# Optimization experiments

Measured on AMD Instinct MI355X. Metric: run time of the kernel, lower is better.

## Reference

```python
import jax, jax.numpy as jnp
import numpy as np

K = 4  # kNN neighbors


def build_edges(density_maps, k):
    B, _, H, W = density_maps.shape
    N = H * W
    flat = density_maps.reshape(B, N)
    # [B, N, N] pairwise absolute density distance
    dist = jnp.abs(flat[:, :, None] - flat[:, None, :])
    # k nearest (excluding self at position 0)
    tgt = jnp.argsort(dist, axis=2)[:, :, 1:k + 1]  # [B, N, k]
    src = jnp.broadcast_to(jnp.arange(N)[None, :, None], (B, N, k))
    offset = (jnp.arange(B) * N)[:, None, None]
    src = (src + offset).reshape(-1)
    tgt = (tgt + offset).reshape(-1)
    n_total = B * N
    loops = jnp.arange(n_total)
    row = jnp.concatenate([src, loops])  # source nodes
    col = jnp.concatenate([tgt, loops])  # target nodes
    return row, col, n_total


def gcn_conv(x, row, col, W, b, n_nodes):
    # symmetric deg^-1/2 normalization, deg computed on target (col)
    deg = jax.ops.segment_sum(jnp.ones_like(col, dtype=x.dtype), col, num_segments=n_nodes)
    dinv = jnp.where(deg > 0, jax.lax.rsqrt(deg), 0.0)
    norm = dinv[row] * dinv[col]  # [E]
    h = x @ W  # transform first, then propagate
    msg = norm[:, None] * h[row]
    out = jax.ops.segment_sum(msg, col, num_segments=n_nodes)
    return out + b


def setup_inputs() -> dict:
    key = jax.random.key(0)
    k1, k2, k3, k4, k5, k6 = jax.random.split(key, 6)
    B, Cin, Chid, Cout, H, W = 4, 256, 512, 256, 64, 64
    density_maps = jax.random.uniform(k1, (B, 1, H, W), dtype=jnp.float32)
    feature_maps = jax.random.normal(k2, (B, Cin, H, W), dtype=jnp.float32)
    W1 = jax.random.normal(k3, (Cin, Chid), dtype=jnp.float32) * (1.0 / np.sqrt(Cin))
    b1 = jnp.zeros((Chid,), dtype=jnp.float32)
    W2 = jax.random.normal(k4, (Chid, Cout), dtype=jnp.float32) * (1.0 / np.sqrt(Chid))
    b2 = jnp.zeros((Cout,), dtype=jnp.float32)
    return {"density_maps": density_maps, "feature_maps": feature_maps,
            "W1": W1, "b1": b1, "W2": W2, "b2": b2}


def reference(density_maps, feature_maps, W1, b1, W2, b2):
    B, Cin, H, Wd = feature_maps.shape
    row, col, n_total = build_edges(density_maps, K)
    # [B,C,H,W] -> [B*H*W, C] node features
    x = feature_maps.transpose(0, 2, 3, 1).reshape(-1, Cin)
    h = jax.nn.relu(gcn_conv(x, row, col, W1, b1, n_total))
    out = jax.nn.relu(gcn_conv(h, row, col, W2, b2, n_total))
    return out.reshape(B, H, Wd, -1).transpose(0, 3, 1, 2)
```

## Files before the change

kernel.cpp:

```cpp
#include <hip/hip_runtime.h>
#include <hip/hip_bf16.h>
#include <stdint.h>

#define N_NODES 16384
#define NPB     4096
#define NB      4
#define KNN     4
#define WIN     12
#define NBUK    4096

typedef short bf16x8 __attribute__((ext_vector_type(8)));
typedef float f32x4 __attribute__((ext_vector_type(4)));
typedef unsigned short u16x8 __attribute__((ext_vector_type(8)));

__device__ __forceinline__ unsigned short f2bf(float f) {
  unsigned u = __float_as_uint(f);
  unsigned r = (u + 0x7fff + ((u >> 16) & 1)) >> 16;
  return (unsigned short)r;
}
__device__ __forceinline__ float bf2f(unsigned short u) {
  return __uint_as_float(((unsigned)u) << 16);
}

__global__ __launch_bounds__(1024)
void bucket_kernel(const float* __restrict__ dm,
                   unsigned long long* __restrict__ skeys_g,
                   int* __restrict__ rank_g,
                   float* __restrict__ dinv_g,
                   unsigned* __restrict__ mask_g) {
  __shared__ int sHist[4096];
  __shared__ int sCur[4096];
  __shared__ unsigned long long sKeys[4096];
  __shared__ unsigned sMask[4096];
  int* part1 = (int*)sKeys;
  int* part2 = (int*)(sKeys + 512);
  const int t = threadIdx.x, b = blockIdx.x;
  const float* d = dm + b * NPB;

  unsigned long long kv[4]; int bk[4];
#pragma unroll
  for (int r = 0; r < 4; ++r) sHist[t + r * 1024] = 0;
  __syncthreads();
#pragma unroll
  for (int r = 0; r < 4; ++r) {
    int i = t + r * 1024;
    float v = d[i];
    kv[r] = (((unsigned long long)__float_as_uint(v)) << 32) | (unsigned)i;
    int k = (int)(v * (float)NBUK); if (k > NBUK - 1) k = NBUK - 1;
    bk[r] = k;
    atomicAdd(&sHist[k], 1);
  }
  __syncthreads();
  int c0 = sHist[4 * t + 0], c1 = sHist[4 * t + 1];
  int c2 = sHist[4 * t + 2], c3 = sHist[4 * t + 3];
  part1[t] = c0 + c1 + c2 + c3;
  __syncthreads();
  if (t < 64) {
    int s = 0;
#pragma unroll
    for (int k = 0; k < 16; ++k) s += part1[16 * t + k];
    part2[t] = s;
  }
  __syncthreads();
  if (t == 0) {
    int a = 0;
    for (int u = 0; u < 64; ++u) { int v = part2[u]; part2[u] = a; a += v; }
  }
  __syncthreads();
  int base = part2[t >> 4];
  for (int k = (t >> 4) * 16; k < t; ++k) base += part1[k];
  sHist[4 * t + 0] = base; sCur[4 * t + 0] = base; base += c0;
  sHist[4 * t + 1] = base; sCur[4 * t + 1] = base; base += c1;
  sHist[4 * t + 2] = base; sCur[4 * t + 2] = base; base += c2;
  sHist[4 * t + 3] = base; sCur[4 * t + 3] = base;
  __syncthreads();
#pragma unroll
  for (int r = 0; r < 4; ++r) {
    int slot = atomicAdd(&sCur[bk[r]], 1);
    sKeys[slot] = kv[r];
  }
  __syncthreads();
#pragma unroll
  for (int r = 0; r < 4; ++r) {
    int g = t + r * 1024;
    int s0 = sHist[g];
    int s1 = (g == NPB - 1) ? NPB : sHist[g + 1];
    for (int i = s0 + 1; i < s1; ++i) {
      unsigned long long x = sKeys[i];
      int j = i - 1;
      while (j >= s0 && sKeys[j] > x) { sKeys[j + 1] = sKeys[j]; --j; }
      sKeys[j + 1] = x;
    }
  }
  __syncthreads();
#pragma unroll
  for (int r = 0; r < 4; ++r) {
    int i = t + r * 1024;
    sHist[i] = 1;
    sMask[i] = 0;
  }
  __syncthreads();
#pragma unroll
  for (int r = 0; r < 4; ++r) {
    int p = t + r * 1024;
    unsigned long long kp = sKeys[p];
    float di = __uint_as_float((unsigned)(kp >> 32));
    int lo = p - WIN; if (lo < 0) lo = 0;
    int hi = p + WIN; if (hi > NPB - 1) hi = NPB - 1;
    unsigned long long k0 = ~0ull, k1 = ~0ull, k2 = ~0ull, k3 = ~0ull, k4 = ~0ull;
    for (int q = lo; q <= hi; ++q) {
      unsigned long long key = sKeys[q];
      float v = __uint_as_float((unsigned)(key >> 32));
      float dist = fabsf(di - v);
      unsigned long long dk = (((unsigned long long)__float_as_uint(dist)) << 24) |
                              ((key & 0xfffull) << 12) | (unsigned)q;
      if (dk < k4) {
        if (dk < k0)      { k4 = k3; k3 = k2; k2 = k1; k1 = k0; k0 = dk; }
        else if (dk < k1) { k4 = k3; k3 = k2; k2 = k1; k1 = dk; }
        else if (dk < k2) { k4 = k3; k3 = k2; k2 = dk; }
        else if (dk < k3) { k4 = k3; k3 = dk; }
        else              { k4 = dk; }
      }
    }
    int t0 = (int)(k1 & 0xfff), t1 = (int)(k2 & 0xfff);
    int t2 = (int)(k3 & 0xfff), t3 = (int)(k4 & 0xfff);
    atomicAdd(&sHist[t0], 1); atomicOr(&sMask[t0], 1u << (p - t0 + WIN));
    atomicAdd(&sHist[t1], 1); atomicOr(&sMask[t1], 1u << (p - t1 + WIN));
    atomicAdd(&sHist[t2], 1); atomicOr(&sMask[t2], 1u << (p - t2 + WIN));
    atomicAdd(&sHist[t3], 1); atomicOr(&sMask[t3], 1u << (p - t3 + WIN));
  }
  __syncthreads();
#pragma unroll
  for (int r = 0; r < 4; ++r) {
    int i = t + r * 1024;
    unsigned long long k = sKeys[i];
    skeys_g[b * NPB + i] = k;
    rank_g[b * NPB + (int)(k & 0xffffffffull)] = i;
    dinv_g[b * NPB + i] = rsqrtf((float)sHist[i]);
    mask_g[b * NPB + i] = sMask[i];
  }
}

__global__ void cvt_all_kernel(const float* __restrict__ fm, unsigned short* __restrict__ px0,
                               const float* __restrict__ W1, unsigned short* __restrict__ W1t,
                               const float* __restrict__ W2, unsigned short* __restrict__ W2t,
                               const int* __restrict__ rank) {
  __shared__ float tile[64][33];
  int z = blockIdx.z;
  const float* in; unsigned short* outbase; int Rin, Cin, r0, c0;
  bool perm = false;
  if (z < NB) {
    in = fm + (size_t)z * 256 * 4096; outbase = px0 + (size_t)z * NPB * 256;
    Rin = 256; Cin = 4096; perm = true;
    c0 = blockIdx.x * 32; r0 = blockIdx.y * 64;
  } else {
    int id = blockIdx.y * 128 + blockIdx.x;
    if (id < 64)       { in = W1; outbase = W1t; Rin = 256; Cin = 512; c0 = (id & 15) * 32; r0 = (id >> 4) * 64; }
    else if (id < 128) { id -= 64; in = W2; outbase = W2t; Rin = 512; Cin = 256; c0 = (id & 7) * 32; r0 = (id >> 3) * 64; }
    else return;
  }
  int tx = threadIdx.x & 31, ty = threadIdx.x >> 5;
  const float* ip = in + (size_t)(r0 + ty) * Cin + c0 + tx;
#pragma unroll
  for (int i = 0; i < 8; ++i) tile[ty + 8 * i][tx] = ip[(size_t)(8 * i) * Cin];
  __syncthreads();
  int orow = threadIdx.x >> 3;
  int oseg = (threadIdx.x & 7) * 8;
  int outrow = c0 + orow;
  if (perm) outrow = rank[(size_t)z * NPB + outrow];
  unsigned short* op = outbase + (size_t)outrow * Rin + r0 + oseg;
  u16x8 o;
#pragma unroll
  for (int k = 0; k < 8; ++k) o[k] = f2bf(tile[oseg + k][orow]);
  *(u16x8*)op = o;
}

__global__ __launch_bounds__(256)
void transpose64_kernel(const float* __restrict__ in, float* __restrict__ out) {
  __shared__ float tile[64][68];
  int cb = blockIdx.x * 64;
  int nb = blockIdx.y * 64;
  int b = blockIdx.z;
  int r = threadIdx.x >> 2, q = threadIdx.x & 3;
  const float* ip = in + ((size_t)b * NPB + nb + r) * 256 + cb;
#pragma unroll
  for (int it = 0; it < 4; ++it) {
    int c = q * 4 + it * 16;
    *(float4*)&tile[r][c] = *(const float4*)(ip + c);
  }
  __syncthreads();
  float* op = out + ((size_t)b * 256 + cb + r) * 4096 + nb;
#pragma unroll
  for (int it = 0; it < 4; ++it) {
    int n = q * 4 + it * 16;
    float4 v;
    v.x = tile[n + 0][r]; v.y = tile[n + 1][r];
    v.z = tile[n + 2][r]; v.w = tile[n + 3][r];
    *(float4*)(op + n) = v;
  }
}

__global__ void prop_kernel(const unsigned short* __restrict__ in,
                            unsigned short* __restrict__ out,
                            const unsigned* __restrict__ mask,
                            const float* __restrict__ dinv) {
  int i = blockIdx.x * 8 + (threadIdx.x >> 5);
  int l = threadIdx.x & 31;
  unsigned m = mask[i];
  float a[8] = {};
#pragma unroll
  for (int off = 0; off < 2 * WIN + 1; ++off) {
    int c = ((m >> off) & 1) + (off == WIN);
    if (c) {
      int q = i + off - WIN;
      float dj = (float)c * dinv[q];
      u16x8 u = *(const u16x8*)(in + (size_t)q * 256 + l * 8);
#pragma unroll
      for (int k = 0; k < 8; ++k) a[k] = fmaf(dj, bf2f(u[k]), a[k]);
    }
  }
  float di = dinv[i];
  u16x8 o;
#pragma unroll
  for (int k = 0; k < 8; ++k) o[k] = f2bf(a[k] * di);
  *(u16x8*)(out + (size_t)i * 256 + l * 8) = o;
}

__global__ void prop2_kernel(const unsigned short* __restrict__ in,
                             float* __restrict__ out,
                             const unsigned* __restrict__ mask,
                             const float* __restrict__ dinv,
                             const float* __restrict__ bias,
                             const unsigned long long* __restrict__ skeys) {
  int i = blockIdx.x * 8 + (threadIdx.x >> 5);
  int l = threadIdx.x & 31;
  unsigned m = mask[i];
  float a[8] = {};
#pragma unroll
  for (int off = 0; off < 2 * WIN + 1; ++off) {
    int c = ((m >> off) & 1) + (off == WIN);
    if (c) {
      int q = i + off - WIN;
      float dj = (float)c * dinv[q];
      u16x8 u = *(const u16x8*)(in + (size_t)q * 256 + l * 8);
#pragma unroll
      for (int k = 0; k < 8; ++k) a[k] = fmaf(dj, bf2f(u[k]), a[k]);
    }
  }
  float di = dinv[i];
  int node = (i & ~(NPB - 1)) + (int)(skeys[i] & 0xffffffffull);
  float4 o0, o1;
  o0.x = fmaxf(a[0] * di + bias[l * 8 + 0], 0.f);
  o0.y = fmaxf(a[1] * di + bias[l * 8 + 1], 0.f);
  o0.z = fmaxf(a[2] * di + bias[l * 8 + 2], 0.f);
  o0.w = fmaxf(a[3] * di + bias[l * 8 + 3], 0.f);
  o1.x = fmaxf(a[4] * di + bias[l * 8 + 4], 0.f);
  o1.y = fmaxf(a[5] * di + bias[l * 8 + 5], 0.f);
  o1.z = fmaxf(a[6] * di + bias[l * 8 + 6], 0.f);
  o1.w = fmaxf(a[7] * di + bias[l * 8 + 7], 0.f);
  *(float4*)(out + (size_t)node * 256 + l * 8) = o0;
  *(float4*)(out + (size_t)node * 256 + l * 8 + 4) = o1;
}

template <bool BIAS_RELU, bool OUT_BF16, int NI>
__global__ __launch_bounds__(256)
void gemm_bf16_kernel(const unsigned short* __restrict__ A,
                      const unsigned short* __restrict__ Bt,
                      void* __restrict__ C, const float* __restrict__ bias,
                      int M, int N, int K) {
  __shared__ char lds[8192 + NI * 8192];
  const int tid = threadIdx.x;
  const int l = tid & 63, w = tid >> 6;
  const int bm = blockIdx.x * 64, bn = blockIdx.y * (64 * NI);
  f32x4 acc[4][NI] = {};

  for (int k0 = 0; k0 < K; k0 += 64) {
    __syncthreads();
#pragma unroll
    for (int q = 0; q < 2; ++q) {
      int o = q * 4096 + tid * 16;
      int r = o >> 7;
      int gc = ((o >> 4) & 7) ^ (r & 7);
      const char* srcA = (const char*)A + ((size_t)(bm + r) * K + k0) * 2 + gc * 16;
      __builtin_amdgcn_global_load_lds(
          (const __attribute__((address_space(1))) void*)srcA,
          (__attribute__((address_space(3))) void*)(lds + o), 16, 0, 0);
    }
#pragma unroll
    for (int q = 0; q < 2 * NI; ++q) {
      int o = q * 4096 + tid * 16;
      int r = o >> 7;
      int gc = ((o >> 4) & 7) ^ (r & 7);
      const char* srcB = (const char*)Bt + ((size_t)(bn + r) * K + k0) * 2 + gc * 16;
      __builtin_amdgcn_global_load_lds(
          (const __attribute__((address_space(1))) void*)srcB,
          (__attribute__((address_space(3))) void*)(lds + 8192 + o), 16, 0, 0);
    }
    __syncthreads();

#pragma unroll
    for (int kk = 0; kk < 64; kk += 32) {
      bf16x8 af[4], bf[NI];
      int gc = (kk >> 3) + (l >> 4);
#pragma unroll
      for (int mi = 0; mi < 4; ++mi) {
        int r = mi * 16 + (l & 15);
        af[mi] = *(const bf16x8*)(lds + r * 128 + ((gc ^ (r & 7)) << 4));
      }
#pragma unroll
      for (int ni = 0; ni < NI; ++ni) {
        int r = w * (16 * NI) + ni * 16 + (l & 15);
        bf[ni] = *(const bf16x8*)(lds + 8192 + r * 128 + ((gc ^ (r & 7)) << 4));
      }
#pragma unroll
      for (int mi = 0; mi < 4; ++mi)
#pragma unroll
        for (int ni = 0; ni < NI; ++ni)
          acc[mi][ni] = __builtin_amdgcn_mfma_f32_16x16x32_bf16(af[mi], bf[ni],
                                                                acc[mi][ni], 0, 0, 0);
    }
  }

#pragma unroll
  for (int mi = 0; mi < 4; ++mi) {
#pragma unroll
    for (int ni = 0; ni < NI; ++ni) {
      int row0 = bm + mi * 16 + ((l >> 4) << 2);
      int col = bn + w * (16 * NI) + ni * 16 + (l & 15);
      float bv = BIAS_RELU ? bias[col] : 0.f;
      f32x4 v = acc[mi][ni];
#pragma unroll
      for (int r = 0; r < 4; ++r) {
        float val = v[r];
        if (BIAS_RELU) val = fmaxf(val + bv, 0.f);
        if (OUT_BF16)
          ((unsigned short*)C)[(size_t)(row0 + r) * N + col] = f2bf(val);
        else
          ((float*)C)[(size_t)(row0 + r) * N + col] = val;
      }
    }
  }
}

extern "C" void kernel_launch(void* const* d_in, const int* in_sizes, int n_in,
                              void* d_out, int out_size, void* d_ws, size_t ws_size,
                              hipStream_t stream) {
  const float* dm = (const float*)d_in[0];
  const float* fm = (const float*)d_in[1];
  const float* W1 = (const float*)d_in[2];
  const float* b1 = (const float*)d_in[3];
  const float* W2 = (const float*)d_in[4];
  const float* b2 = (const float*)d_in[5];
  float* out = (float*)d_out;

  char* ws = (char*)d_ws;
  float*              dinv  = (float*)(ws + 0x050000);
  unsigned*           mask  = (unsigned*)(ws + 0x060000);
  unsigned long long* skeys = (unsigned long long*)(ws + 0x100000);
  int*                rank  = (int*)(ws + 0x130000);
  unsigned short*     W1t   = (unsigned short*)(ws + 0x190000);
  unsigned short*     W2t   = (unsigned short*)(ws + 0x1D0000);
  unsigned short*     px0   = (unsigned short*)(ws + 0x0400000);
  unsigned short*     px    = (unsigned short*)(ws + 0x0C00000);
  unsigned short*     h1    = (unsigned short*)(ws + 0x1400000);
  unsigned short*     t2    = (unsigned short*)(ws + 0x2400000);
  float*              xout  = (float*)(ws + 0x2C00000);
  (void)ws_size; (void)in_sizes; (void)n_in; (void)out_size;

  bucket_kernel<<<NB, 1024, 0, stream>>>(dm, skeys, rank, dinv, mask);

  cvt_all_kernel<<<dim3(128, 4, NB + 1), 256, 0, stream>>>(fm, px0, W1, W1t, W2, W2t, rank);

  prop_kernel<<<N_NODES / 8, 256, 0, stream>>>(px0, px, mask, dinv);
  gemm_bf16_kernel<true, true, 1><<<dim3(256, 8), 256, 0, stream>>>(
      px, W1t, h1, b1, 16384, 512, 256);

  gemm_bf16_kernel<false, true, 1><<<dim3(256, 4), 256, 0, stream>>>(
      h1, W2t, t2, nullptr, 16384, 256, 512);
  prop2_kernel<<<N_NODES / 8, 256, 0, stream>>>(t2, xout, mask, dinv, b2, skeys);

  transpose64_kernel<<<dim3(4, 64, NB), 256, 0, stream>>>(xout, out);
}
```

Measured before the change: 83.12 us.

## Split kNN window selection out of bucket kernel into a wide separate kernel

Moves the per-node windowed top-k selection out of the 4-block bucket kernel into a new 64-block kernel that reads the sorted keys from global memory and uses global atomics for degree and mask. Degree is stored as an int and rsqrt is recomputed in both propagation kernels instead of storing dinv. The aim is to spread the selection loop, which previously ran on only four workgroups, across more CUs. The cost is an extra launch, global atomics instead of LDS atomics, and repeated rsqrt work.

```diff
diff --git a/kernel.cpp b/kernel.cpp
--- a/kernel.cpp
+++ b/kernel.cpp
@@ -26,12 +26,11 @@
 void bucket_kernel(const float* __restrict__ dm,
                    unsigned long long* __restrict__ skeys_g,
                    int* __restrict__ rank_g,
-                   float* __restrict__ dinv_g,
+                   int* __restrict__ deg_g,
                    unsigned* __restrict__ mask_g) {
   __shared__ int sHist[4096];
   __shared__ int sCur[4096];
   __shared__ unsigned long long sKeys[4096];
-  __shared__ unsigned sMask[4096];
   int* part1 = (int*)sKeys;
   int* part2 = (int*)(sKeys + 512);
   const int t = threadIdx.x, b = blockIdx.x;
@@ -96,49 +95,46 @@
 #pragma unroll
   for (int r = 0; r < 4; ++r) {
     int i = t + r * 1024;
-    sHist[i] = 1;
-    sMask[i] = 0;
-  }
-  __syncthreads();
-#pragma unroll
-  for (int r = 0; r < 4; ++r) {
-    int p = t + r * 1024;
-    unsigned long long kp = sKeys[p];
-    float di = __uint_as_float((unsigned)(kp >> 32));
-    int lo = p - WIN; if (lo < 0) lo = 0;
-    int hi = p + WIN; if (hi > NPB - 1) hi = NPB - 1;
-    unsigned long long k0 = ~0ull, k1 = ~0ull, k2 = ~0ull, k3 = ~0ull, k4 = ~0ull;
-    for (int q = lo; q <= hi; ++q) {
-      unsigned long long key = sKeys[q];
-      float v = __uint_as_float((unsigned)(key >> 32));
-      float dist = fabsf(di - v);
-      unsigned long long dk = (((unsigned long long)__float_as_uint(dist)) << 24) |
-                              ((key & 0xfffull) << 12) | (unsigned)q;
-      if (dk < k4) {
-        if (dk < k0)      { k4 = k3; k3 = k2; k2 = k1; k1 = k0; k0 = dk; }
-        else if (dk < k1) { k4 = k3; k3 = k2; k2 = k1; k1 = dk; }
-        else if (dk < k2) { k4 = k3; k3 = k2; k2 = dk; }
-        else if (dk < k3) { k4 = k3; k3 = dk; }
-        else              { k4 = dk; }
-      }
-    }
-    int t0 = (int)(k1 & 0xfff), t1 = (int)(k2 & 0xfff);
-    int t2 = (int)(k3 & 0xfff), t3 = (int)(k4 & 0xfff);
-    atomicAdd(&sHist[t0], 1); atomicOr(&sMask[t0], 1u << (p - t0 + WIN));
-    atomicAdd(&sHist[t1], 1); atomicOr(&sMask[t1], 1u << (p - t1 + WIN));
-    atomicAdd(&sHist[t2], 1); atomicOr(&sMask[t2], 1u << (p - t2 + WIN));
-    atomicAdd(&sHist[t3], 1); atomicOr(&sMask[t3], 1u << (p - t3 + WIN));
-  }
-  __syncthreads();
-#pragma unroll
-  for (int r = 0; r < 4; ++r) {
-    int i = t + r * 1024;
     unsigned long long k = sKeys[i];
     skeys_g[b * NPB + i] = k;
     rank_g[b * NPB + (int)(k & 0xffffffffull)] = i;
-    dinv_g[b * NPB + i] = rsqrtf((float)sHist[i]);
-    mask_g[b * NPB + i] = sMask[i];
-  }
+    deg_g[b * NPB + i] = 1;
+    mask_g[b * NPB + i] = 0;
+  }
+}
+
+__global__ void select_kernel(const unsigned long long* __restrict__ skeys,
+                              int* __restrict__ deg, unsigned* __restrict__ mask) {
+  int p = blockIdx.x * 256 + threadIdx.x;
+  if (p >= N_NODES) return;
+  int b = p >> 12, pl = p & (NPB - 1);
+  const unsigned long long* sk = skeys + b * NPB;
+  unsigned long long kp = sk[pl];
+  float di = __uint_as_float((unsigned)(kp >> 32));
+  int lo = pl - WIN; if (lo < 0) lo = 0;
+  int hi = pl + WIN; if (hi > NPB - 1) hi = NPB - 1;
+  unsigned long long k0 = ~0ull, k1 = ~0ull, k2 = ~0ull, k3 = ~0ull, k4 = ~0ull;
+  for (int q = lo; q <= hi; ++q) {
+    unsigned long long key = sk[q];
+    float v = __uint_as_float((unsigned)(key >> 32));
+    float dist = fabsf(di - v);
+    unsigned long long dk = (((unsigned long long)__float_as_uint(dist)) << 24) |
+                            ((key & 0xfffull) << 12) | (unsigned)q;
+    if (dk < k4) {
+      if (dk < k0)      { k4 = k3; k3 = k2; k2 = k1; k1 = k0; k0 = dk; }
+      else if (dk < k1) { k4 = k3; k3 = k2; k2 = k1; k1 = dk; }
+      else if (dk < k2) { k4 = k3; k3 = k2; k2 = dk; }
+      else if (dk < k3) { k4 = k3; k3 = dk; }
+      else              { k4 = dk; }
+    }
+  }
+  int base = b * NPB;
+  int t0 = (int)(k1 & 0xfff), t1 = (int)(k2 & 0xfff);
+  int t2 = (int)(k3 & 0xfff), t3 = (int)(k4 & 0xfff);
+  atomicAdd(&deg[base + t0], 1); atomicOr(&mask[base + t0], 1u << (pl - t0 + WIN));
+  atomicAdd(&deg[base + t1], 1); atomicOr(&mask[base + t1], 1u << (pl - t1 + WIN));
+  atomicAdd(&deg[base + t2], 1); atomicOr(&mask[base + t2], 1u << (pl - t2 + WIN));
+  atomicAdd(&deg[base + t3], 1); atomicOr(&mask[base + t3], 1u << (pl - t3 + WIN));
 }
 
 __global__ void cvt_all_kernel(const float* __restrict__ fm, unsigned short* __restrict__ px0,
@@ -203,7 +199,7 @@
 __global__ void prop_kernel(const unsigned short* __restrict__ in,
                             unsigned short* __restrict__ out,
                             const unsigned* __restrict__ mask,
-                            const float* __restrict__ dinv) {
+                            const int* __restrict__ deg) {
   int i = blockIdx.x * 8 + (threadIdx.x >> 5);
   int l = threadIdx.x & 31;
   unsigned m = mask[i];
@@ -213,13 +209,13 @@
     int c = ((m >> off) & 1) + (off == WIN);
     if (c) {
       int q = i + off - WIN;
-      float dj = (float)c * dinv[q];
+      float dj = (float)c * rsqrtf((float)deg[q]);
       u16x8 u = *(const u16x8*)(in + (size_t)q * 256 + l * 8);
 #pragma unroll
       for (int k = 0; k < 8; ++k) a[k] = fmaf(dj, bf2f(u[k]), a[k]);
     }
   }
-  float di = dinv[i];
+  float di = rsqrtf((float)deg[i]);
   u16x8 o;
 #pragma unroll
   for (int k = 0; k < 8; ++k) o[k] = f2bf(a[k] * di);
@@ -229,7 +225,7 @@
 __global__ void prop2_kernel(const unsigned short* __restrict__ in,
                              float* __restrict__ out,
                              const unsigned* __restrict__ mask,
-                             const float* __restrict__ dinv,
+                             const int* __restrict__ deg,
                              const float* __restrict__ bias,
                              const unsigned long long* __restrict__ skeys) {
   int i = blockIdx.x * 8 + (threadIdx.x >> 5);
@@ -241,13 +237,13 @@
     int c = ((m >> off) & 1) + (off == WIN);
     if (c) {
       int q = i + off - WIN;
-      float dj = (float)c * dinv[q];
+      float dj = (float)c * rsqrtf((float)deg[q]);
       u16x8 u = *(const u16x8*)(in + (size_t)q * 256 + l * 8);
 #pragma unroll
       for (int k = 0; k < 8; ++k) a[k] = fmaf(dj, bf2f(u[k]), a[k]);
     }
   }
-  float di = dinv[i];
+  float di = rsqrtf((float)deg[i]);
   int node = (i & ~(NPB - 1)) + (int)(skeys[i] & 0xffffffffull);
   float4 o0, o1;
   o0.x = fmaxf(a[0] * di + bias[l * 8 + 0], 0.f);
@@ -354,7 +350,7 @@
   float* out = (float*)d_out;
 
   char* ws = (char*)d_ws;
-  float*              dinv  = (float*)(ws + 0x050000);
+  int*                deg   = (int*)(ws + 0x040000);
   unsigned*           mask  = (unsigned*)(ws + 0x060000);
   unsigned long long* skeys = (unsigned long long*)(ws + 0x100000);
   int*                rank  = (int*)(ws + 0x130000);
@@ -367,17 +363,18 @@
   float*              xout  = (float*)(ws + 0x2C00000);
   (void)ws_size; (void)in_sizes; (void)n_in; (void)out_size;
 
-  bucket_kernel<<<NB, 1024, 0, stream>>>(dm, skeys, rank, dinv, mask);
+  bucket_kernel<<<NB, 1024, 0, stream>>>(dm, skeys, rank, deg, mask);
+  select_kernel<<<64, 256, 0, stream>>>(skeys, deg, mask);
 
   cvt_all_kernel<<<dim3(128, 4, NB + 1), 256, 0, stream>>>(fm, px0, W1, W1t, W2, W2t, rank);
 
-  prop_kernel<<<N_NODES / 8, 256, 0, stream>>>(px0, px, mask, dinv);
+  prop_kernel<<<N_NODES / 8, 256, 0, stream>>>(px0, px, mask, deg);
   gemm_bf16_kernel<true, true, 1><<<dim3(256, 8), 256, 0, stream>>>(
       px, W1t, h1, b1, 16384, 512, 256);
 
   gemm_bf16_kernel<false, true, 1><<<dim3(256, 4), 256, 0, stream>>>(
       h1, W2t, t2, nullptr, 16384, 256, 512);
-  prop2_kernel<<<N_NODES / 8, 256, 0, stream>>>(t2, xout, mask, dinv, b2, skeys);
+  prop2_kernel<<<N_NODES / 8, 256, 0, stream>>>(t2, xout, mask, deg, b2, skeys);
 
   transpose64_kernel<<<dim3(4, 64, NB), 256, 0, stream>>>(xout, out);
 }
```

After: 76.50 us. 1.09x faster.
